# Kernel optimization log

Measured on AMD Instinct MI355X. Metric: run time of the kernel, lower is better.

## Reference

```python
import jax, jax.numpy as jnp
import numpy as np

B, T, LD, PD, W, NL = 2048, 256, 32, 8, 64, 3
TH, CH = LD * 2, W * 2  # token/channel mixing hidden dims (expansion=2)


def setup_inputs() -> dict:
    key = jax.random.key(0)
    ks = jax.random.split(key, 12)
    n = lambda k, s, sc=0.02: jax.random.normal(k, s, jnp.float32) * sc
    return {
        "phys": jax.random.normal(ks[0], (B, T, PD), jnp.float32),
        "latents": jax.random.uniform(ks[1], (B, LD), jnp.float32),
        "pos_emb": n(ks[2], (1, LD, W)),
        "tokW": n(ks[3], (1, W)), "tokb": jnp.zeros((W,), jnp.float32),
        "physW1": n(ks[4], (PD, W)), "physb1": jnp.zeros((W,), jnp.float32),
        "physW2": n(ks[5], (W, W)), "physb2": jnp.zeros((W,), jnp.float32),
        "tn_g": jnp.ones((NL, W), jnp.float32), "tn_b": jnp.zeros((NL, W), jnp.float32),
        "tiW": n(ks[6], (NL, LD, TH)), "tib": jnp.zeros((NL, TH), jnp.float32),
        "toW": n(ks[7], (NL, TH, LD)), "tob": jnp.zeros((NL, LD), jnp.float32),
        "cn_g": jnp.ones((NL, W), jnp.float32), "cn_b": jnp.zeros((NL, W), jnp.float32),
        "ciW": n(ks[8], (NL, W, CH)), "cib": jnp.zeros((NL, CH), jnp.float32),
        "coW": n(ks[9], (NL, CH, W)), "cob": jnp.zeros((NL, W), jnp.float32),
        "hn_g": jnp.ones((W,), jnp.float32), "hn_b": jnp.zeros((W,), jnp.float32),
        "headW": n(ks[10], (W, 1), 0.0002),  # 0.02 init * 0.01 scaling from torch
        "headb": jnp.zeros((1,), jnp.float32),
    }


def _ln(x, g, b):
    m = jnp.mean(x, -1, keepdims=True)
    v = jnp.mean((x - m) ** 2, -1, keepdims=True)
    return (x - m) * jax.lax.rsqrt(v + 1e-5) * g + b


def reference(phys, latents, pos_emb, tokW, tokb, physW1, physb1, physW2, physb2,
              tn_g, tn_b, tiW, tib, toW, tob, cn_g, cn_b, ciW, cib, coW, cob,
              hn_g, hn_b, headW, headb):
    gelu = lambda x: jax.nn.gelu(x, approximate=False)  # torch nn.GELU default (exact)

    def step(current, phys_t):
        # token_projection of current[..., None]: Linear(1, W)
        tokens = current[:, :, None] * tokW[0] + tokb  # [B, LD, W]
        p = gelu(phys_t @ physW1 + physb1) @ physW2 + physb2  # [B, W]
        tokens = tokens + p[:, None, :] + pos_emb
        for i in range(NL):
            # token mixing: LN over width, mix across latent tokens
            mt = jnp.swapaxes(_ln(tokens, tn_g[i], tn_b[i]), 1, 2)  # [B, W, LD]
            mt = gelu(mt @ tiW[i] + tib[i]) @ toW[i] + tob[i]       # [B, W, LD]
            tokens = tokens + jnp.swapaxes(mt, 1, 2)
            # channel mixing over width
            mc = _ln(tokens, cn_g[i], cn_b[i])
            tokens = tokens + (gelu(mc @ ciW[i] + cib[i]) @ coW[i] + cob[i])
        delta = (_ln(tokens, hn_g, hn_b) @ headW + headb)[..., 0]  # [B, LD]
        new = jnp.clip(current + delta, 0.0, 1.0)
        return new, new

    _, outs = jax.lax.scan(step, latents, jnp.swapaxes(phys, 0, 1))  # [T, B, LD]
    return jnp.swapaxes(outs, 0, 1)  # [B, T, LD]
```

## Files before the change

kernel.cpp:

```cpp
#include <hip/hip_runtime.h>
#include <math.h>


namespace {
constexpr int Tt = 256, NL = 3;

typedef float    f32x4 __attribute__((ext_vector_type(4)));
typedef _Float16 half2 __attribute__((ext_vector_type(2)));
typedef _Float16 h16x4 __attribute__((ext_vector_type(4)));
typedef _Float16 h16x8 __attribute__((ext_vector_type(8)));

#define MFMA32(a, b, c) __builtin_amdgcn_mfma_f32_16x16x32_f16((a), (b), (c), 0, 0, 0)
#define MFMA16(a, b, c) __builtin_amdgcn_mfma_f32_16x16x16f16((a), (b), (c), 0, 0, 0)
#define REL(p, v) __hip_atomic_store((p), (v), __ATOMIC_RELEASE, __HIP_MEMORY_SCOPE_WORKGROUP)
#define ACQ(p) __hip_atomic_load((p), __ATOMIC_ACQUIRE, __HIP_MEMORY_SCOPE_WORKGROUP)

__device__ __forceinline__ half2 h2c(float v) { return (half2)((_Float16)v); }
__device__ __forceinline__ f32x4 f4s(float v) { return (f32x4)v; }
__device__ __forceinline__ half2 pkrtz(float a, float b) {
    return __builtin_bit_cast(half2, __builtin_amdgcn_cvt_pkrtz(a, b));
}
__device__ __forceinline__ void st4h(short* p, half2 a, half2 b) {
    uint2 v;
    v.x = __builtin_bit_cast(unsigned int, a);
    v.y = __builtin_bit_cast(unsigned int, b);
    *(uint2*)p = v;
}
__device__ __forceinline__ h16x4 h4(half2 a, half2 b) {
    h16x4 v; v[0] = a[0]; v[1] = a[1]; v[2] = b[0]; v[3] = b[1]; return v;
}
__device__ __forceinline__ half2 lo2(h16x4 v) { half2 r; r[0] = v[0]; r[1] = v[1]; return r; }
__device__ __forceinline__ half2 hi2(h16x4 v) { half2 r; r[0] = v[2]; r[1] = v[3]; return r; }
__device__ __forceinline__ half2 gelu_pk(half2 x) {
    half2 tc = __builtin_elementwise_min(__builtin_elementwise_max(x, h2c(-3.0f)), h2c(3.0f));
    half2 s = (tc * tc) * h2c(0.125f);
    half2 p = s * h2c(0.1455169f) + h2c(-0.446340f);
    p = s * p + h2c(0.604927f);
    p = s * p + h2c(-0.529702f);
    p = s * p + h2c(0.3989423f);
    return x * (h2c(0.5f) + tc * p);
}
__device__ __forceinline__ float gelu_f(float x) {
    float tc = fminf(fmaxf(x, -3.f), 3.f);
    float s = tc * tc;
    float p = fmaf(s, 3.55266e-5f, -8.71758e-4f);
    p = fmaf(s, p, 9.45198e-3f);
    p = fmaf(s, p, -6.62128e-2f);
    p = fmaf(s, p, 0.3989423f);
    return x * fmaf(tc, p, 0.5f);
}
__device__ __forceinline__ float rowsum16(float x) {
    x += __builtin_bit_cast(float, __builtin_amdgcn_update_dpp(0, __builtin_bit_cast(int, x), 0x121, 0xf, 0xf, false));
    x += __builtin_bit_cast(float, __builtin_amdgcn_update_dpp(0, __builtin_bit_cast(int, x), 0x122, 0xf, 0xf, false));
    x += __builtin_bit_cast(float, __builtin_amdgcn_update_dpp(0, __builtin_bit_cast(int, x), 0x124, 0xf, 0xf, false));
    x += __builtin_bit_cast(float, __builtin_amdgcn_update_dpp(0, __builtin_bit_cast(int, x), 0x128, 0xf, 0xf, false));
    return x;
}
__device__ __forceinline__ short f2h(float x) {
    return __builtin_bit_cast(short, (_Float16)x);
}

__global__ void lno_prep(const float* __restrict__ tiW, const float* __restrict__ toW,
                         const float* __restrict__ ciW, const float* __restrict__ coW,
                         const float* __restrict__ physW2, short* __restrict__ wsf) {
    int id = blockIdx.x * 256 + threadIdx.x;
    if (id < 6144) {
        int e = id & 255, tile = id >> 8;
        int lane = e >> 2, j = e & 3;
        int q = lane >> 4, cc = lane & 15;
        int kc = tile & 1, u = (tile >> 1) & 3, il = tile >> 3;
        wsf[id] = f2h(tiW[il * 2048 + (16 * kc + 4 * q + j) * 64 + 16 * u + cc]);
    } else if (id < 12288) {
        int t = id - 6144;
        int e = t & 255, tile = t >> 8;
        int lane = e >> 2, j = e & 3;
        int q = lane >> 4, cc = lane & 15;
        int kc = tile & 3, sb = (tile >> 2) & 1, il = tile >> 3;
        wsf[id] = f2h(toW[il * 2048 + (16 * kc + 4 * q + j) * 32 + 16 * sb + cc]);
    } else if (id < 36864) {
        int t = id - 12288;
        int j = t & 7, lane = (t >> 3) & 63, g = t >> 9;
        int il = g >> 4, mtc = (g >> 1) & 7, ks = g & 1;
        int m = mtc * 16 + (lane & 15), k = ks * 32 + (lane >> 4) * 8 + j;
        wsf[id] = f2h(ciW[il * 8192 + k * 128 + m]);
    } else if (id < 61440) {
        int t = id - 36864;
        int j = t & 7, lane = (t >> 3) & 63, g = t >> 9;
        int il = g >> 4, nt = (g >> 2) & 3, ks = g & 3;
        int n = nt * 16 + (lane & 15), k = ks * 32 + (lane >> 4) * 8 + j;
        wsf[id] = f2h(coW[il * 8192 + k * 64 + n]);
    } else if (id < 65536) {
        int t = id - 61440;
        int w = t >> 6, k = t & 63;
        ((float*)(wsf + 61440))[t] = physW2[k * 64 + w];
    }
}

__global__ void lno_phys(const float* __restrict__ phys, const float* __restrict__ physW1,
                         const float* __restrict__ physb1, const float* __restrict__ physW2,
                         const float* __restrict__ physb2, short* __restrict__ pout) {
    __shared__ float hsh[4][64];
    const int lane = threadIdx.x & 63, wv = threadIdx.x >> 6;
    const size_t bt = (size_t)blockIdx.x * 4 + wv;
    const float* pt = phys + bt * 8;
    float4 px0 = *(const float4*)pt, px1 = *(const float4*)(pt + 4);
    float a = physb1[lane];
    a = fmaf(px0.x, physW1[0 * 64 + lane], a);
    a = fmaf(px0.y, physW1[1 * 64 + lane], a);
    a = fmaf(px0.z, physW1[2 * 64 + lane], a);
    a = fmaf(px0.w, physW1[3 * 64 + lane], a);
    a = fmaf(px1.x, physW1[4 * 64 + lane], a);
    a = fmaf(px1.y, physW1[5 * 64 + lane], a);
    a = fmaf(px1.z, physW1[6 * 64 + lane], a);
    a = fmaf(px1.w, physW1[7 * 64 + lane], a);
    hsh[wv][lane] = gelu_f(a);
    float acc = physb2[lane];
#pragma unroll
    for (int k = 0; k < 64; ++k) acc = fmaf(hsh[wv][k], physW2[k * 64 + lane], acc);
    pout[bt * 64 + (lane & 15) * 4 + (lane >> 4)] = f2h(acc);
}

__global__ __launch_bounds__(1024, 4) void lno_scan(
    const float* __restrict__ latents, const float* __restrict__ pos_emb,
    const float* __restrict__ tokW,    const float* __restrict__ tokb,
    const float* __restrict__ tn_g,    const float* __restrict__ tn_b,
    const float* __restrict__ tib,     const float* __restrict__ tob,
    const float* __restrict__ cn_g,    const float* __restrict__ cn_b,
    const float* __restrict__ cib,     const float* __restrict__ cob,
    const float* __restrict__ hn_g,    const float* __restrict__ hn_b,
    const float* __restrict__ headW,   const float* __restrict__ headb,
    const short* __restrict__ wsf,     const short* pbuf, float* out)
{
    __shared__ __align__(16) short wAll[61440];
    __shared__ __align__(16) short tbuf[8][2048];
    __shared__ __align__(16) float biasL[1632];
    __shared__ int flags[8][8];

    const int tid = threadIdx.x, lane = tid & 63, wv = tid >> 6;
    const int sb = wv & 1, tm = wv >> 1, pn = sb ^ 1;
    const int q = lane >> 4, c = lane & 15;
    const int b = blockIdx.x * 8 + tm;
    short* buf = tbuf[tm];
    short* mysc = buf + sb * 1024;
    int* F = flags[tm];

    const short* A1L = wAll;
    const short* A2L = wAll + 6144;
    const short* A3L = wAll + 12288;
    const short* B4L = wAll + 36864;

    if (wv < 15) {
        const unsigned int* src = (const unsigned int*)wsf;
#pragma unroll
        for (int i = 0; i < 8; ++i) {
            const int cid = wv * 8 + i;
            __builtin_amdgcn_global_load_lds(src + cid * 256 + lane * 4,
                                             (unsigned int*)&wAll[cid * 512], 16, 0, 0);
        }
    }
    for (int i = tid; i < 192; i += 1024) {
        biasL[i] = tib[i];
        biasL[672 + i]  = tn_g[i];
        biasL[864 + i]  = tn_b[i];
        biasL[1056 + i] = cn_g[i];
        biasL[1248 + i] = cn_b[i];
        biasL[1440 + i] = cob[i];
    }
    for (int i = tid; i < 96;  i += 1024) biasL[192 + i] = tob[i];
    for (int i = tid; i < 384; i += 1024) biasL[288 + i] = cib[i];
    if (tid < 64) ((int*)flags)[tid] = 0;

    float tokw_r[4], tokb_r[4], gh_r[4];
#pragma unroll
    for (int nt = 0; nt < 4; ++nt) {
        tokw_r[nt] = tokW[nt * 16 + c];
        tokb_r[nt] = tokb[nt * 16 + c];
        gh_r[nt]   = hn_g[nt * 16 + c] * headW[nt * 16 + c];
    }
    float bhp = 0.f;
#pragma unroll
    for (int nt = 0; nt < 4; ++nt) bhp = fmaf(hn_b[nt * 16 + c], headW[nt * 16 + c], bhp);
    const float bh = rowsum16(bhp) + headb[0];

    f32x4 pe4[4];
#pragma unroll
    for (int nt = 0; nt < 4; ++nt)
#pragma unroll
        for (int r = 0; r < 4; ++r)
            pe4[nt][r] = pos_emb[(sb * 16 + q * 4 + r) * 64 + nt * 16 + c];

    f32x4 cur = *(const f32x4*)(latents + b * 32 + sb * 16 + q * 4);
    f32x4 tok[4];

    __syncthreads();

    auto stats = [&](f32x4& mean, f32x4& rsig) {
        f32x4 s4 = (tok[0] + tok[1]) + (tok[2] + tok[3]);
        f32x4 q4 = tok[0] * tok[0];
        q4 = __builtin_elementwise_fma(tok[1], tok[1], q4);
        q4 = __builtin_elementwise_fma(tok[2], tok[2], q4);
        q4 = __builtin_elementwise_fma(tok[3], tok[3], q4);
#pragma unroll
        for (int r = 0; r < 4; ++r) {
            float ss = rowsum16(s4[r]);
            float qq = rowsum16(q4[r]);
            float m = ss * 0.015625f;
            float v = fmaf(-m, m, qq * 0.015625f);
            mean[r] = m;
            rsig[r] = __builtin_amdgcn_rsqf(v + 1e-5f);
        }
    };

    const short* pb = pbuf + (size_t)b * Tt * 64 + c * 4;
    h16x4 pvc = *(const h16x4*)pb;

#pragma unroll 1
    for (int t = 0; t < Tt; ++t) {
        const h16x4 pv = pvc;
        if (t + 1 < Tt) pvc = *(const h16x4*)(pb + (t + 1) * 64);

#pragma unroll
        for (int nt = 0; nt < 4; ++nt) {
            const f32x4 bp = f4s(tokb_r[nt] + (float)pv[nt]);
            tok[nt] = __builtin_elementwise_fma(cur, f4s(tokw_r[nt]), pe4[nt] + bp);
        }

#pragma unroll 1
        for (int il = 0; il < NL; ++il) {
            const int g = t * 3 + il + 1;
            f32x4 mean, rsig;
            stats(mean, rsig);
            h16x4 b1own[4];
#pragma unroll
            for (int nt = 0; nt < 4; ++nt) {
                const float tng = biasL[672 + il * 64 + nt * 16 + c];
                const float tnb = biasL[864 + il * 64 + nt * 16 + c];
                f32x4 y = __builtin_elementwise_fma((tok[nt] - mean) * rsig,
                                                    f4s(tng), f4s(tnb));
                half2 d0 = pkrtz(y[0], y[1]), d1 = pkrtz(y[2], y[3]);
                b1own[nt] = h4(d0, d1);
                st4h(&buf[sb * 1024 + (nt * 64 + lane) * 4], d0, d1);
            }
            if (lane == 0) REL(&F[sb], g);
            {
                const f32x4 tb = *(const f32x4*)&biasL[192 + il * 32 + sb * 16 + q * 4];
#pragma unroll
                for (int nt = 0; nt < 4; ++nt) tok[nt] += tb;
            }
            f32x4 hacc[2][4];
#pragma unroll
            for (int uu = 0; uu < 2; ++uu) {
                const int u = 2 * sb + uu;
                const h16x4 a1 = *(const h16x4*)(A1L + (((il * 4 + u) * 2) + sb) * 256 + lane * 4);
                const f32x4 bi = *(const f32x4*)&biasL[il * 64 + u * 16 + q * 4];
#pragma unroll
                for (int nt = 0; nt < 4; ++nt) hacc[uu][nt] = MFMA16(a1, b1own[nt], bi);
            }
            while (ACQ(&F[pn]) < g) {}
            h16x4 b1p[4];
#pragma unroll
            for (int nt = 0; nt < 4; ++nt)
                b1p[nt] = *(const h16x4*)&buf[pn * 1024 + (nt * 64 + lane) * 4];
#pragma unroll
            for (int uu = 0; uu < 2; ++uu) {
                const int u = 2 * sb + uu;
                const h16x4 a1 = *(const h16x4*)(A1L + (((il * 4 + u) * 2) + pn) * 256 + lane * 4);
#pragma unroll
                for (int nt = 0; nt < 4; ++nt) hacc[uu][nt] = MFMA16(a1, b1p[nt], hacc[uu][nt]);
            }
            if (sb == 1 && lane == 0) REL(&F[5], g);
            h16x4 b2own[2][4];
#pragma unroll
            for (int uu = 0; uu < 2; ++uu)
#pragma unroll
                for (int nt = 0; nt < 4; ++nt) {
                    half2 e0 = gelu_pk(pkrtz(hacc[uu][nt][0], hacc[uu][nt][1]));
                    half2 e1 = gelu_pk(pkrtz(hacc[uu][nt][2], hacc[uu][nt][3]));
                    b2own[uu][nt] = h4(e0, e1);
                }
            if (sb == 0) {
                while (ACQ(&F[5]) < g) {}
#pragma unroll
                for (int uu = 0; uu < 2; ++uu)
#pragma unroll
                    for (int nt = 0; nt < 4; ++nt)
                        st4h(&buf[((uu * 4 + nt) * 64 + lane) * 4], lo2(b2own[uu][nt]), hi2(b2own[uu][nt]));
                if (lane == 0) REL(&F[2], g);
#pragma unroll
                for (int kc = 0; kc < 2; ++kc) {
                    const h16x4 a2 = *(const h16x4*)(A2L + ((il * 2 + sb) * 4 + kc) * 256 + lane * 4);
#pragma unroll
                    for (int nt = 0; nt < 4; ++nt) tok[nt] = MFMA16(a2, b2own[kc][nt], tok[nt]);
                }
                while (ACQ(&F[3]) < g) {}
#pragma unroll
                for (int kc = 2; kc < 4; ++kc) {
                    const h16x4 a2 = *(const h16x4*)(A2L + ((il * 2 + sb) * 4 + kc) * 256 + lane * 4);
#pragma unroll
                    for (int nt = 0; nt < 4; ++nt) {
                        const h16x4 b2p = *(const h16x4*)&buf[(((kc - 2) * 4 + nt) * 64 + lane) * 4];
                        tok[nt] = MFMA16(a2, b2p, tok[nt]);
                    }
                }
                if (lane == 0) REL(&F[4], g);
            } else {
#pragma unroll
                for (int kcl = 0; kcl < 2; ++kcl) {
                    const int kc = 2 + kcl;
                    const h16x4 a2 = *(const h16x4*)(A2L + ((il * 2 + sb) * 4 + kc) * 256 + lane * 4);
#pragma unroll
                    for (int nt = 0; nt < 4; ++nt) tok[nt] = MFMA16(a2, b2own[kcl][nt], tok[nt]);
                }
                while (ACQ(&F[2]) < g) {}
#pragma unroll
                for (int kc = 0; kc < 2; ++kc) {
                    const h16x4 a2 = *(const h16x4*)(A2L + ((il * 2 + sb) * 4 + kc) * 256 + lane * 4);
#pragma unroll
                    for (int nt = 0; nt < 4; ++nt) {
                        const h16x4 b2p = *(const h16x4*)&buf[((kc * 4 + nt) * 64 + lane) * 4];
                        tok[nt] = MFMA16(a2, b2p, tok[nt]);
                    }
                }
#pragma unroll
                for (int uu = 0; uu < 2; ++uu)
#pragma unroll
                    for (int nt = 0; nt < 4; ++nt)
                        st4h(&buf[((uu * 4 + nt) * 64 + lane) * 4], lo2(b2own[uu][nt]), hi2(b2own[uu][nt]));
                if (lane == 0) REL(&F[3], g);
            }

            stats(mean, rsig);
            if (sb == 1) { while (ACQ(&F[4]) < g) {} }
#pragma unroll
            for (int nt = 0; nt < 4; ++nt) {
                const float cng = biasL[1056 + il * 64 + nt * 16 + c];
                const float cnb = biasL[1248 + il * 64 + nt * 16 + c];
#pragma unroll
                for (int r = 0; r < 4; ++r) {
                    float v = fmaf((tok[nt][r] - mean[r]) * rsig[r], cng, cnb);
                    mysc[((nt >> 1) * 64 + (2 * (nt & 1) + (c >> 3)) * 16 + 4 * q + r) * 8 + (c & 7)] = f2h(v);
                }
            }
            h16x8 b3[2];
#pragma unroll
            for (int kc = 0; kc < 2; ++kc) b3[kc] = *(const h16x8*)&mysc[(kc * 64 + lane) * 8];
#pragma unroll
            for (int nt = 0; nt < 4; ++nt) tok[nt] += f4s(biasL[1440 + il * 64 + nt * 16 + c]);
#pragma unroll
            for (int hh = 0; hh < 2; ++hh) {
#pragma unroll
                for (int mm = 0; mm < 4; ++mm) {
                    const int mtc = hh * 4 + mm;
                    const h16x8 a30 = *(const h16x8*)(A3L + il * 8192 + (mtc * 2 + 0) * 512 + lane * 8);
                    const h16x8 a31 = *(const h16x8*)(A3L + il * 8192 + (mtc * 2 + 1) * 512 + lane * 8);
                    const f32x4 bi3 = *(const f32x4*)&biasL[288 + il * 128 + mtc * 16 + q * 4];
                    f32x4 acc = MFMA32(a30, b3[0], bi3);
                    acc = MFMA32(a31, b3[1], acc);
                    st4h(&mysc[(((mtc >> 1) & 1) * 64 + ((mtc & 1) * 2 + (q >> 1)) * 16 + c) * 8 + (q & 1) * 4],
                         gelu_pk(pkrtz(acc[0], acc[1])), gelu_pk(pkrtz(acc[2], acc[3])));
                }
                h16x8 a4[2];
#pragma unroll
                for (int kf = 0; kf < 2; ++kf) a4[kf] = *(const h16x8*)&mysc[(kf * 64 + lane) * 8];
#pragma unroll
                for (int nt = 0; nt < 4; ++nt) {
                    const h16x8 b40 = *(const h16x8*)(B4L + il * 8192 + (nt * 4 + hh * 2 + 0) * 512 + lane * 8);
                    const h16x8 b41 = *(const h16x8*)(B4L + il * 8192 + (nt * 4 + hh * 2 + 1) * 512 + lane * 8);
                    tok[nt] = MFMA32(a4[0], b40, tok[nt]);
                    tok[nt] = MFMA32(a4[1], b41, tok[nt]);
                }
            }
        }

        {
            f32x4 mean, rsig;
            stats(mean, rsig);
            f32x4 l4 = (tok[0] - mean) * f4s(gh_r[0]);
            l4 = __builtin_elementwise_fma(tok[1] - mean, f4s(gh_r[1]), l4);
            l4 = __builtin_elementwise_fma(tok[2] - mean, f4s(gh_r[2]), l4);
            l4 = __builtin_elementwise_fma(tok[3] - mean, f4s(gh_r[3]), l4);
            f32x4 ls;
#pragma unroll
            for (int r = 0; r < 4; ++r) ls[r] = rowsum16(l4[r]);
            f32x4 nv = cur + __builtin_elementwise_fma(rsig, ls, f4s(bh));
            nv = __builtin_elementwise_min(__builtin_elementwise_max(nv, f4s(0.f)), f4s(1.f));
            cur = nv;
            if (c == 0)
                *(f32x4*)(out + ((size_t)b * Tt + t) * 32 + sb * 16 + q * 4) = cur;
        }
    }
}
}

extern "C" void kernel_launch(void* const* d_in, const int* in_sizes, int n_in,
                              void* d_out, int out_size, void* d_ws, size_t ws_size,
                              hipStream_t stream) {
    (void)in_sizes; (void)n_in; (void)ws_size; (void)out_size;
    const float* phys    = (const float*)d_in[0];
    const float* latents = (const float*)d_in[1];
    const float* pos_emb = (const float*)d_in[2];
    const float* tokW    = (const float*)d_in[3];
    const float* tokb    = (const float*)d_in[4];
    const float* physW1  = (const float*)d_in[5];
    const float* physb1  = (const float*)d_in[6];
    const float* physW2  = (const float*)d_in[7];
    const float* physb2  = (const float*)d_in[8];
    const float* tn_g    = (const float*)d_in[9];
    const float* tn_b    = (const float*)d_in[10];
    const float* tiW     = (const float*)d_in[11];
    const float* tib     = (const float*)d_in[12];
    const float* toW     = (const float*)d_in[13];
    const float* tob     = (const float*)d_in[14];
    const float* cn_g    = (const float*)d_in[15];
    const float* cn_b    = (const float*)d_in[16];
    const float* ciW     = (const float*)d_in[17];
    const float* cib     = (const float*)d_in[18];
    const float* coW     = (const float*)d_in[19];
    const float* cob     = (const float*)d_in[20];
    const float* hn_g    = (const float*)d_in[21];
    const float* hn_b    = (const float*)d_in[22];
    const float* headW   = (const float*)d_in[23];
    const float* headb   = (const float*)d_in[24];

    lno_prep<<<dim3(256), dim3(256), 0, stream>>>(tiW, toW, ciW, coW, physW2, (short*)d_ws);
    lno_phys<<<dim3(131072), dim3(256), 0, stream>>>(phys, physW1, physb1, physW2, physb2,
                                                     (short*)d_out);
    lno_scan<<<dim3(256), dim3(1024), 0, stream>>>(
        latents, pos_emb, tokW, tokb, tn_g, tn_b, tib, tob,
        cn_g, cn_b, cib, cob, hn_g, hn_b, headW, headb,
        (const short*)d_ws, (const short*)d_out, (float*)d_out);
}
```

Measured before the change: 7.246 ms.

## Cut register pressure: fp16 pos-emb, fused MFMA+GELU, relax launch bounds

```diff
diff --git a/kernel.cpp b/kernel.cpp
--- a/kernel.cpp
+++ b/kernel.cpp
@@ -120,7 +120,7 @@
     pout[bt * 64 + (lane & 15) * 4 + (lane >> 4)] = f2h(acc);
 }
 
-__global__ __launch_bounds__(1024, 4) void lno_scan(
+__global__ __launch_bounds__(1024, 2) void lno_scan(
     const float* __restrict__ latents, const float* __restrict__ pos_emb,
     const float* __restrict__ tokW,    const float* __restrict__ tokb,
     const float* __restrict__ tn_g,    const float* __restrict__ tn_b,
@@ -170,11 +170,10 @@
     for (int i = tid; i < 384; i += 1024) biasL[288 + i] = cib[i];
     if (tid < 64) ((int*)flags)[tid] = 0;
 
-    float tokw_r[4], tokb_r[4], gh_r[4];
+    float tokw_r[4], gh_r[4];
 #pragma unroll
     for (int nt = 0; nt < 4; ++nt) {
         tokw_r[nt] = tokW[nt * 16 + c];
-        tokb_r[nt] = tokb[nt * 16 + c];
         gh_r[nt]   = hn_g[nt * 16 + c] * headW[nt * 16 + c];
     }
     float bhp = 0.f;
@@ -182,12 +181,15 @@
     for (int nt = 0; nt < 4; ++nt) bhp = fmaf(hn_b[nt * 16 + c], headW[nt * 16 + c], bhp);
     const float bh = rowsum16(bhp) + headb[0];
 
-    f32x4 pe4[4];
-#pragma unroll
-    for (int nt = 0; nt < 4; ++nt)
-#pragma unroll
-        for (int r = 0; r < 4; ++r)
-            pe4[nt][r] = pos_emb[(sb * 16 + q * 4 + r) * 64 + nt * 16 + c];
+    h16x4 peh[4];
+#pragma unroll
+    for (int r = 0; r < 4; ++r) {
+        float v0 = pos_emb[(sb * 16 + q * 4 + r) * 64 +  0 + c] + tokb[ 0 + c];
+        float v1 = pos_emb[(sb * 16 + q * 4 + r) * 64 + 16 + c] + tokb[16 + c];
+        float v2 = pos_emb[(sb * 16 + q * 4 + r) * 64 + 32 + c] + tokb[32 + c];
+        float v3 = pos_emb[(sb * 16 + q * 4 + r) * 64 + 48 + c] + tokb[48 + c];
+        peh[r] = h4(pkrtz(v0, v1), pkrtz(v2, v3));
+    }
 
     f32x4 cur = *(const f32x4*)(latents + b * 32 + sb * 16 + q * 4);
     f32x4 tok[4];
@@ -219,10 +221,16 @@
         const h16x4 pv = pvc;
         if (t + 1 < Tt) pvc = *(const h16x4*)(pb + (t + 1) * 64);
 
-#pragma unroll
-        for (int nt = 0; nt < 4; ++nt) {
-            const f32x4 bp = f4s(tokb_r[nt] + (float)pv[nt]);
-            tok[nt] = __builtin_elementwise_fma(cur, f4s(tokw_r[nt]), pe4[nt] + bp);
+        {
+            f32x4 pvx;
+#pragma unroll
+            for (int nt = 0; nt < 4; ++nt) pvx[nt] = (float)pv[nt];
+#pragma unroll
+            for (int r = 0; r < 4; ++r) {
+#pragma unroll
+                for (int nt = 0; nt < 4; ++nt)
+                    tok[nt][r] = fmaf(cur[r], tokw_r[nt], (float)peh[r][nt] + pvx[nt]);
+            }
         }
 
 #pragma unroll 1
@@ -247,37 +255,28 @@
 #pragma unroll
                 for (int nt = 0; nt < 4; ++nt) tok[nt] += tb;
             }
-            f32x4 hacc[2][4];
+            while (ACQ(&F[pn]) < g) {}
+            h16x4 b1p[4];
+#pragma unroll
+            for (int nt = 0; nt < 4; ++nt)
+                b1p[nt] = *(const h16x4*)&buf[pn * 1024 + (nt * 64 + lane) * 4];
+            if (sb == 1 && lane == 0) REL(&F[5], g);
+            h16x4 b2own[2][4];
 #pragma unroll
             for (int uu = 0; uu < 2; ++uu) {
                 const int u = 2 * sb + uu;
-                const h16x4 a1 = *(const h16x4*)(A1L + (((il * 4 + u) * 2) + sb) * 256 + lane * 4);
+                const h16x4 a1o = *(const h16x4*)(A1L + (((il * 4 + u) * 2) + sb) * 256 + lane * 4);
+                const h16x4 a1p = *(const h16x4*)(A1L + (((il * 4 + u) * 2) + pn) * 256 + lane * 4);
                 const f32x4 bi = *(const f32x4*)&biasL[il * 64 + u * 16 + q * 4];
 #pragma unroll
-                for (int nt = 0; nt < 4; ++nt) hacc[uu][nt] = MFMA16(a1, b1own[nt], bi);
-            }
-            while (ACQ(&F[pn]) < g) {}
-            h16x4 b1p[4];
-#pragma unroll
-            for (int nt = 0; nt < 4; ++nt)
-                b1p[nt] = *(const h16x4*)&buf[pn * 1024 + (nt * 64 + lane) * 4];
-#pragma unroll
-            for (int uu = 0; uu < 2; ++uu) {
-                const int u = 2 * sb + uu;
-                const h16x4 a1 = *(const h16x4*)(A1L + (((il * 4 + u) * 2) + pn) * 256 + lane * 4);
-#pragma unroll
-                for (int nt = 0; nt < 4; ++nt) hacc[uu][nt] = MFMA16(a1, b1p[nt], hacc[uu][nt]);
-            }
-            if (sb == 1 && lane == 0) REL(&F[5], g);
-            h16x4 b2own[2][4];
-#pragma unroll
-            for (int uu = 0; uu < 2; ++uu)
-#pragma unroll
                 for (int nt = 0; nt < 4; ++nt) {
-                    half2 e0 = gelu_pk(pkrtz(hacc[uu][nt][0], hacc[uu][nt][1]));
-                    half2 e1 = gelu_pk(pkrtz(hacc[uu][nt][2], hacc[uu][nt][3]));
+                    f32x4 hv = MFMA16(a1o, b1own[nt], bi);
+                    hv = MFMA16(a1p, b1p[nt], hv);
+                    half2 e0 = gelu_pk(pkrtz(hv[0], hv[1]));
+                    half2 e1 = gelu_pk(pkrtz(hv[2], hv[3]));
                     b2own[uu][nt] = h4(e0, e1);
                 }
+            }
             if (sb == 0) {
                 while (ACQ(&F[5]) < g) {}
 #pragma unroll
```

New measurement: 6.649 ms. -8.2%, faster.
